# Kernel optimization log

Measured on AMD Instinct MI355X. Metric: run time of the kernel, lower is better.

The kernel has to match this reference:

```python
import jax, jax.numpy as jnp
import numpy as np

POLY_Q = 2.0  # normalizer='poly_2'
N_HEADS = 12
LN_EPS = 1e-5  # torch nn.LayerNorm default


def poly_norm(x, q=POLY_Q):
    # Newton solve for c such that sum_k 1/(-x-c)^q == 1, row-wise (last axis).
    c = jnp.min(-x, axis=-1, keepdims=True) - 1.0  # ensures -x - c >= 1
    for _ in range(6):
        base = -x - c
        poly_sum = jnp.sum(base ** (-q), axis=-1, keepdims=True)
        poly_sum_der = q * jnp.sum(base ** (-(q + 1.0)), axis=-1, keepdims=True)
        c = c - (poly_sum - 1.0) / (poly_sum_der + 1e-8)
    return (-x - c) ** (-q)


def layer_norm(x, g, b, eps=LN_EPS):
    m = jnp.mean(x, axis=-1, keepdims=True)
    v = jnp.mean((x - m) ** 2, axis=-1, keepdims=True)
    return (x - m) * jax.lax.rsqrt(v + eps) * g + b


def setup_inputs() -> dict:
    key = jax.random.key(0)
    B, S, D, M = 2, 1024, 768, 3072
    ks = jax.random.split(key, 8)
    sd = 1.0 / np.sqrt(D)
    sm = 1.0 / np.sqrt(M)
    return {
        "x": jax.random.normal(ks[0], (B, S, D), dtype=jnp.float32),
        "ln1_g": jnp.ones((D,), jnp.float32),
        "ln1_b": jnp.zeros((D,), jnp.float32),
        "wq": jax.random.normal(ks[1], (D, D), jnp.float32) * sd,
        "bq": jnp.zeros((D,), jnp.float32),
        "wk": jax.random.normal(ks[2], (D, D), jnp.float32) * sd,
        "bk": jnp.zeros((D,), jnp.float32),
        "wv": jax.random.normal(ks[3], (D, D), jnp.float32) * sd,
        "bv": jnp.zeros((D,), jnp.float32),
        "wo": jax.random.normal(ks[4], (D, D), jnp.float32) * sd,
        "bo": jnp.zeros((D,), jnp.float32),
        "ln2_g": jnp.ones((D,), jnp.float32),
        "ln2_b": jnp.zeros((D,), jnp.float32),
        "w1": jax.random.normal(ks[5], (D, M), jnp.float32) * sd,
        "b1": jnp.zeros((M,), jnp.float32),
        "w2": jax.random.normal(ks[6], (M, D), jnp.float32) * sm,
        "b2": jnp.zeros((D,), jnp.float32),
    }


def reference(x, ln1_g, ln1_b, wq, bq, wk, bk, wv, bv, wo, bo,
              ln2_g, ln2_b, w1, b1, w2, b2):
    B, S, D = x.shape
    H = N_HEADS
    Dh = D // H
    # --- pre-LN self-attention with poly normalizer ---
    y = layer_norm(x, ln1_g, ln1_b)
    q = (y @ wq + bq).reshape(B, S, H, Dh) / jnp.sqrt(jnp.float32(Dh))
    k = (y @ wk + bk).reshape(B, S, H, Dh)
    v = (y @ wv + bv).reshape(B, S, H, Dh)
    scores = jnp.einsum('bqhd,bkhd->bhqk', q, k)  # [B,H,S,S]
    attn_w = poly_norm(scores)
    attn = jnp.einsum('bhqk,bkhd->bqhd', attn_w, v).reshape(B, S, D)
    x1 = x + attn @ wo + bo  # residual 1
    # --- MLP block ---
    y2 = layer_norm(x1, ln2_g, ln2_b)
    h = jax.nn.gelu(y2 @ w1 + b1, approximate=False)  # torch GELU = exact erf
    out = x1 + h @ w2 + b2  # residual 2
    return out
```

## Files before the change

kernel.cpp:

```cpp
#include <hip/hip_runtime.h>

#define DEV __device__ __forceinline__

typedef unsigned short u16;
typedef __attribute__((ext_vector_type(8))) short bf16x8;
typedef __attribute__((ext_vector_type(4))) float f32x4;
typedef __attribute__((ext_vector_type(4))) unsigned int u32x4;

DEV u16 f2bf(float f) {
  union { float f; unsigned u; } un; un.f = f;
  unsigned r = un.u + 0x7fffu + ((un.u >> 16) & 1u);
  return (u16)(r >> 16);
}

DEV void gload16(const void* g, void* l) {
  __builtin_amdgcn_global_load_lds((const __attribute__((address_space(1))) void*)g,
                                   (__attribute__((address_space(3))) void*)l, 16, 0, 0);
}

template <int N>
DEV void vm_wait() { asm volatile("s_waitcnt vmcnt(%0)" :: "n"(N) : "memory"); }

DEV float blk_sum(float v, volatile float* sb) {
#pragma unroll
  for (int o = 32; o; o >>= 1) v += __shfl_xor(v, o);
  __syncthreads();
  if ((threadIdx.x & 63) == 0) sb[threadIdx.x >> 6] = v;
  __syncthreads();
  return sb[0] + sb[1] + sb[2] + sb[3];
}

__global__ __launch_bounds__(256) void ln_kernel(const float* __restrict__ x,
                                                 const float* __restrict__ g,
                                                 const float* __restrict__ b,
                                                 u16* __restrict__ y) {
  __shared__ float sb[4];
  const size_t row = blockIdx.x;
  const float* xr = x + row * 768;
  const int t = threadIdx.x;
  float v0 = xr[t], v1 = xr[t + 256], v2 = xr[t + 512];
  float mean = blk_sum(v0 + v1 + v2, sb) * (1.0f / 768.0f);
  float d0 = v0 - mean, d1 = v1 - mean, d2 = v2 - mean;
  float var = blk_sum(d0 * d0 + d1 * d1 + d2 * d2, sb) * (1.0f / 768.0f);
  float inv = rsqrtf(var + 1e-5f);
  u16* yr = y + row * 768;
  yr[t]       = f2bf(d0 * inv * g[t]       + b[t]);
  yr[t + 256] = f2bf(d1 * inv * g[t + 256] + b[t + 256]);
  yr[t + 512] = f2bf(d2 * inv * g[t + 512] + b[t + 512]);
}

__global__ __launch_bounds__(256) void wt_transpose(const float* __restrict__ in,
                                                    u16* __restrict__ out, int K, int N) {
  __shared__ float tile[32][33];
  const int tx = threadIdx.x & 31, ty = threadIdx.x >> 5;
  const int n0 = blockIdx.x * 32, k0 = blockIdx.y * 32;
#pragma unroll
  for (int i = 0; i < 4; i++)
    tile[ty + 8 * i][tx] = in[(size_t)(k0 + ty + 8 * i) * N + n0 + tx];
  __syncthreads();
#pragma unroll
  for (int i = 0; i < 4; i++)
    out[(size_t)(n0 + ty + 8 * i) * K + k0 + tx] = f2bf(tile[tx][ty + 8 * i]);
}

__global__ __launch_bounds__(256) void v_transpose(const u16* __restrict__ qkv,
                                                   u16* __restrict__ vT) {
  __shared__ u16 tile[32][33];
  const int tx = threadIdx.x & 31, ty = threadIdx.x >> 5;
  const int z = blockIdx.z, b = z / 12, h = z % 12;
  const int s0 = blockIdx.x * 32, d0 = blockIdx.y * 32;
#pragma unroll
  for (int i = 0; i < 4; i++)
    tile[ty + 8 * i][tx] =
        qkv[(size_t)(b * 1024 + s0 + ty + 8 * i) * 2304 + 1536 + h * 64 + d0 + tx];
  __syncthreads();
#pragma unroll
  for (int i = 0; i < 4; i++)
    vT[(size_t)(z * 64 + d0 + ty + 8 * i) * 1024 + s0 + tx] = tile[tx][ty + 8 * i];
}

__global__ __launch_bounds__(512) void fused_attn(const u16* __restrict__ qkv,
                                                  const u16* __restrict__ vT,
                                                  u16* __restrict__ attn) {
  __shared__ __align__(16) u16 wlds[16 * 1024];

  const int tid = threadIdx.x;
  const int w = tid >> 6, l = tid & 63;
  const int g = l >> 4, lr = l & 15;
  const int bh = blockIdx.y, b = bh / 12, h = bh % 12;
  const int q0 = blockIdx.x * 16;

  const u16* qrow = qkv + (size_t)(b * 1024 + q0 + lr) * 2304 + h * 64;
  const u16* krow = qkv + (size_t)(b * 1024 + w * 128 + lr) * 2304 + 768 + h * 64;

  bf16x8 af[2];
  af[0] = *(const bf16x8*)(qrow + g * 8);
  af[1] = *(const bf16x8*)(qrow + 32 + g * 8);

  f32x4 acc[8];
#pragma unroll
  for (int n = 0; n < 8; n++) acc[n] = (f32x4){0.f, 0.f, 0.f, 0.f};

#pragma unroll
  for (int n = 0; n < 8; n++) {
    bf16x8 b0 = *(const bf16x8*)(krow + n * 16 * 2304 + g * 8);
    bf16x8 b1 = *(const bf16x8*)(krow + n * 16 * 2304 + 32 + g * 8);
    acc[n] = __builtin_amdgcn_mfma_f32_16x16x32_bf16(af[0], b0, acc[n], 0, 0, 0);
    acc[n] = __builtin_amdgcn_mfma_f32_16x16x32_bf16(af[1], b1, acc[n], 0, 0, 0);
  }

#pragma unroll
  for (int n = 0; n < 8; n++)
#pragma unroll
    for (int r = 0; r < 4; r++) {
      int row = g * 4 + r;
      int col = w * 128 + n * 16 + lr;
      unsigned off = (unsigned)(row * 2048 + col * 2);
      off ^= (unsigned)(row & 7) << 4;
      *(u16*)((char*)wlds + off) = f2bf(acc[n][r]);
    }
  __syncthreads();

  const int crow = tid >> 5, l32 = tid & 31;
  const unsigned cswz = (unsigned)(crow & 7) << 4;
  const unsigned cbase = (unsigned)(crow * 2048 + l32 * 64);
  float xs[32];
#pragma unroll
  for (int j = 0; j < 4; j++) {
    u32x4 raw = *(const u32x4*)((const char*)wlds + ((cbase + j * 16u) ^ cswz));
#pragma unroll
    for (int e = 0; e < 4; e++) {
      union { unsigned u; float f; } lo, hi;
      lo.u = raw[e] << 16;
      hi.u = raw[e] & 0xffff0000u;
      xs[j * 8 + e * 2] = lo.f;
      xs[j * 8 + e * 2 + 1] = hi.f;
    }
  }

  float mx = xs[0];
#pragma unroll
  for (int i = 1; i < 32; i++) mx = fmaxf(mx, xs[i]);
#pragma unroll
  for (int o = 1; o < 32; o <<= 1) mx = fmaxf(mx, __shfl_xor(mx, o));
  float c = -mx - 1.0f;

#pragma unroll 1
  for (int it = 0; it < 6; it++) {
    float s2 = 0.f, s3 = 0.f;
#pragma unroll
    for (int i = 0; i < 32; i++) {
      float rr = __builtin_amdgcn_rcpf(-(xs[i] + c));
      float r2 = rr * rr;
      s2 += r2;
      s3 = fmaf(r2, rr, s3);
    }
#pragma unroll
    for (int o = 1; o < 32; o <<= 1) {
      s2 += __shfl_xor(s2, o);
      s3 += __shfl_xor(s3, o);
    }
    c -= (s2 - 1.0f) * __builtin_amdgcn_rcpf(2.0f * s3 + 1e-8f);
  }

#pragma unroll
  for (int j = 0; j < 4; j++) {
    u32x4 outv;
#pragma unroll
    for (int e = 0; e < 4; e++) {
      float r0 = __builtin_amdgcn_rcpf(-(xs[j * 8 + e * 2] + c));
      float r1 = __builtin_amdgcn_rcpf(-(xs[j * 8 + e * 2 + 1] + c));
      outv[e] = (unsigned)f2bf(r0 * r0) | ((unsigned)f2bf(r1 * r1) << 16);
    }
    *(u32x4*)((char*)wlds + ((cbase + j * 16u) ^ cswz)) = outv;
  }
  __syncthreads();

  if (w < 4) {
    const int nf = w;
    const u16* vrow = vT + (size_t)(bh * 64 + nf * 16 + lr) * 1024;
    const unsigned swz = (unsigned)(lr & 7) << 4;
    const unsigned abase = (unsigned)(lr * 2048);
    f32x4 oacc = (f32x4){0.f, 0.f, 0.f, 0.f};
#pragma unroll
    for (int ks = 0; ks < 32; ks++) {
      bf16x8 afr = *(const bf16x8*)((const char*)wlds +
                                    ((abase + (unsigned)(ks * 64 + g * 16)) ^ swz));
      bf16x8 bfr = *(const bf16x8*)(vrow + ks * 32 + g * 8);
      oacc = __builtin_amdgcn_mfma_f32_16x16x32_bf16(afr, bfr, oacc, 0, 0, 0);
    }
    u16* orow = attn + (size_t)(b * 1024 + q0 + g * 4) * 768 + h * 64 + nf * 16 + lr;
#pragma unroll
    for (int r = 0; r < 4; r++) orow[(size_t)r * 768] = f2bf(oacc[r]);
  }
}

__global__ __launch_bounds__(256) void splitk_reduce(const float* __restrict__ p,
                                                     const float* __restrict__ bias,
                                                     const float* __restrict__ res,
                                                     float* __restrict__ out) {
  const size_t S = 2048ull * 768;
  size_t i = ((size_t)blockIdx.x * 256 + threadIdx.x) * 4;
  f32x4 v = *(const f32x4*)&p[i];
  v += *(const f32x4*)&p[i + S];
  v += *(const f32x4*)&p[i + 2 * S];
  v += *(const f32x4*)&p[i + 3 * S];
  int col = (int)(i % 768);
  v += *(const f32x4*)&bias[col];
  v += *(const f32x4*)&res[i];
  *(f32x4*)&out[i] = v;
}

template <int BM, int WN, int EPI>
__global__ __launch_bounds__(256) void gemm_bt(
    const u16* __restrict__ A, int lda, long long sAb, long long sAh,
    const u16* __restrict__ B0, const u16* __restrict__ B1, const u16* __restrict__ B2,
    int ldb, long long sBb, long long sBh,
    void* __restrict__ Cv, int ldc, long long sCb, long long sCh,
    const float* __restrict__ bias0, const float* __restrict__ bias1,
    const float* __restrict__ bias2, const float* __restrict__ res, int K) {
  constexpr int WCOL = (BM == 128) ? 2 : 4;
  constexpr int BN = WCOL * WN * 16;
  constexpr int NA = BM / 64;
  constexpr int NB = BN / 64;
  constexpr int LT = NA + NB;
  __shared__ __align__(16) u16 lds_a[3][BM * 32];
  __shared__ __align__(16) u16 lds_b[3][BN * 32];

  const int zb = blockIdx.z / 12, zh = blockIdx.z % 12;
  A += zb * sAb + zh * sAh;

  const int colbase = blockIdx.y * BN;
  const u16* B = B0;
  const float* bias = bias0;
  int biasoff = 0;
  float qscale = 1.0f;
  if (EPI == 0) {
    int sel = colbase / 768;
    B = (sel == 0) ? B0 : ((sel == 1) ? B1 : B2);
    bias = (sel == 0) ? bias0 : ((sel == 1) ? bias1 : bias2);
    biasoff = sel * 768;
    qscale = (sel == 0) ? 0.125f : 1.0f;
  }
  B += zb * sBb + zh * sBh;

  const int tid = threadIdx.x;
  const size_t ldab = (size_t)lda * 2, ldbb = (size_t)ldb * 2;
  const char* Abase = (const char*)(A + (size_t)blockIdx.x * BM * lda);
  const char* Bbase = (const char*)(B + (size_t)(colbase - biasoff) * ldb);

  const char* ap[NA];
  const char* bp[NB];
#pragma unroll
  for (int j = 0; j < NA; j++) {
    int lin = (j * 256 + tid) * 16;
    ap[j] = Abase + (size_t)(lin >> 6) * ldab + (lin & 63);
  }
#pragma unroll
  for (int j = 0; j < NB; j++) {
    int lin = (j * 256 + tid) * 16;
    bp[j] = Bbase + (size_t)(lin >> 6) * ldbb + (lin & 63);
  }

  auto stage = [&](int buf) {
#pragma unroll
    for (int j = 0; j < NA; j++) {
      gload16(ap[j], (char*)&lds_a[buf][0] + (j * 256 + tid) * 16);
      ap[j] += 64;
    }
#pragma unroll
    for (int j = 0; j < NB; j++) {
      gload16(bp[j], (char*)&lds_b[buf][0] + (j * 256 + tid) * 16);
      bp[j] += 64;
    }
  };

  f32x4 acc[4][WN];
#pragma unroll
  for (int m = 0; m < 4; m++)
#pragma unroll
    for (int n = 0; n < WN; n++) acc[m][n] = (f32x4){0.f, 0.f, 0.f, 0.f};

  const int w = tid >> 6, l = tid & 63;
  const int wm = (BM == 128) ? (w >> 1) : 0;
  const int wn = (BM == 128) ? (w & 1) : w;
  const int lr = l & 15, kg = l >> 4;

  const int nt = K / 32;
  stage(0);
  if (nt > 1) stage(1);

  for (int t = 0; t < nt; ++t) {
    const int buf = t % 3;
    if (t + 2 < nt) {
      stage((t + 2) % 3);
      vm_wait<2 * LT>();
    } else if (t + 1 < nt) {
      vm_wait<LT>();
    } else {
      vm_wait<0>();
    }
    __builtin_amdgcn_sched_barrier(0);
    __builtin_amdgcn_s_barrier();
    __builtin_amdgcn_sched_barrier(0);

    bf16x8 af[4], bfr[WN];
#pragma unroll
    for (int m = 0; m < 4; m++)
      af[m] = *(const bf16x8*)&lds_a[buf][(wm * 64 + m * 16 + lr) * 32 + kg * 8];
#pragma unroll
    for (int n = 0; n < WN; n++)
      bfr[n] = *(const bf16x8*)&lds_b[buf][(wn * WN * 16 + n * 16 + lr) * 32 + kg * 8];
#pragma unroll
    for (int m = 0; m < 4; m++)
#pragma unroll
      for (int n = 0; n < WN; n++)
        acc[m][n] = __builtin_amdgcn_mfma_f32_16x16x32_bf16(af[m], bfr[n], acc[m][n], 0, 0, 0);

    __builtin_amdgcn_sched_barrier(0);
    __builtin_amdgcn_s_barrier();
    __builtin_amdgcn_sched_barrier(0);
  }

  const int row0 = blockIdx.x * BM + ((BM == 128) ? wm * 64 : 0) + kg * 4;
  const int colb = colbase + wn * WN * 16;
  float* Cf = (float*)Cv + (size_t)zb * sCb + (size_t)zh * sCh;
  u16* Cu = (u16*)Cv + (size_t)zb * sCb + (size_t)zh * sCh;
#pragma unroll
  for (int m = 0; m < 4; m++) {
#pragma unroll
    for (int n = 0; n < WN; n++) {
#pragma unroll
      for (int r = 0; r < 4; r++) {
        int row = row0 + m * 16 + r;
        int col = colb + n * 16 + lr;
        size_t idx = (size_t)row * ldc + col;
        float v = acc[m][n][r];
        if (EPI == 0) {
          Cu[idx] = f2bf((v + bias[col - biasoff]) * qscale);
        } else if (EPI == 1) {
          Cf[idx] = v;
        } else if (EPI == 2) {
          Cu[idx] = f2bf(v);
        } else if (EPI == 3) {
          Cf[idx] = v + bias[col] + res[idx];
        } else {
          v += bias[col];
          Cu[idx] = f2bf(0.5f * v * (1.0f + erff(v * 0.70710678118654752f)));
        }
      }
    }
  }
}

extern "C" void kernel_launch(void* const* d_in, const int* in_sizes, int n_in,
                              void* d_out, int out_size, void* d_ws, size_t ws_size,
                              hipStream_t stream) {
  const float* x     = (const float*)d_in[0];
  const float* ln1_g = (const float*)d_in[1];
  const float* ln1_b = (const float*)d_in[2];
  const float* wq    = (const float*)d_in[3];
  const float* bq    = (const float*)d_in[4];
  const float* wk    = (const float*)d_in[5];
  const float* bk    = (const float*)d_in[6];
  const float* wv    = (const float*)d_in[7];
  const float* bv    = (const float*)d_in[8];
  const float* wo    = (const float*)d_in[9];
  const float* bo    = (const float*)d_in[10];
  const float* ln2_g = (const float*)d_in[11];
  const float* ln2_b = (const float*)d_in[12];
  const float* w1    = (const float*)d_in[13];
  const float* b1    = (const float*)d_in[14];
  const float* w2    = (const float*)d_in[15];
  const float* b2    = (const float*)d_in[16];
  float* out = (float*)d_out;

  char* p = (char*)d_ws;
  auto alloc = [&](size_t n) { char* r = p; p += (n + 255) & ~(size_t)255; return r; };
  u16*   qkv    = (u16*)  alloc(2048ull * 2304 * 2);
  u16*   y1     = (u16*)  alloc(2048ull * 768 * 2);
  u16*   vT     = (u16*)  alloc(24ull * 64 * 1024 * 2);
  u16*   attn   = (u16*)  alloc(2048ull * 768 * 2);
  float* x1     = (float*)alloc(2048ull * 768 * 4);
  u16*   y2     = (u16*)  alloc(2048ull * 768 * 2);
  u16*   hbuf   = (u16*)  alloc(2048ull * 3072 * 2);
  float* pbuf   = (float*)alloc(4ull * 2048 * 768 * 4);
  u16*   wq_t   = (u16*)  alloc(768ull * 768 * 2);
  u16*   wk_t   = (u16*)  alloc(768ull * 768 * 2);
  u16*   wv_t   = (u16*)  alloc(768ull * 768 * 2);
  u16*   wo_t   = (u16*)  alloc(768ull * 768 * 2);
  u16*   w1_t   = (u16*)  alloc(3072ull * 768 * 2);
  u16*   w2_t   = (u16*)  alloc(768ull * 3072 * 2);
  (void)in_sizes; (void)n_in; (void)out_size; (void)ws_size;

  wt_transpose<<<dim3(24, 24), 256, 0, stream>>>(wq, wq_t, 768, 768);
  wt_transpose<<<dim3(24, 24), 256, 0, stream>>>(wk, wk_t, 768, 768);
  wt_transpose<<<dim3(24, 24), 256, 0, stream>>>(wv, wv_t, 768, 768);
  wt_transpose<<<dim3(24, 24), 256, 0, stream>>>(wo, wo_t, 768, 768);
  wt_transpose<<<dim3(96, 24), 256, 0, stream>>>(w1, w1_t, 768, 3072);
  wt_transpose<<<dim3(24, 96), 256, 0, stream>>>(w2, w2_t, 3072, 768);

  ln_kernel<<<2048, 256, 0, stream>>>(x, ln1_g, ln1_b, y1);

  gemm_bt<128, 4, 0><<<dim3(16, 18, 1), 256, 0, stream>>>(
      y1, 768, 0, 0, wq_t, wk_t, wv_t, 768, 0, 0, qkv, 2304, 0, 0, bq, bk, bv, nullptr, 768);

  v_transpose<<<dim3(32, 2, 24), 256, 0, stream>>>(qkv, vT);

  fused_attn<<<dim3(64, 24), 512, 0, stream>>>(qkv, vT, attn);

  gemm_bt<64, 2, 3><<<dim3(32, 6, 1), 256, 0, stream>>>(
      attn, 768, 0, 0, wo_t, nullptr, nullptr, 768, 0, 0, x1, 768, 0, 0,
      bo, nullptr, nullptr, x, 768);

  ln_kernel<<<2048, 256, 0, stream>>>(x1, ln2_g, ln2_b, y2);

  gemm_bt<128, 4, 4><<<dim3(16, 24, 1), 256, 0, stream>>>(
      y2, 768, 0, 0, w1_t, nullptr, nullptr, 768, 0, 0, hbuf, 3072, 0, 0,
      b1, nullptr, nullptr, nullptr, 768);

  gemm_bt<64, 2, 1><<<dim3(32, 6, 4), 256, 0, stream>>>(
      hbuf, 3072, 0, 768LL, w2_t, nullptr, nullptr, 3072, 0, 768LL,
      pbuf, 768, 0, 1572864LL, nullptr, nullptr, nullptr, nullptr, 768);

  splitk_reduce<<<1536, 256, 0, stream>>>(pbuf, b2, x1, out);
}
```

Baseline: 182.7 us.

## Merge weight transposes into one launch and fuse V transpose into QKV epilogue

Replaces six separate weight-transpose launches with one kernel that maps a flat block index to the right weight matrix. It also removes the V-transpose kernel: the QKV GEMM's V-column blocks now write bias-added V directly in transposed [b,h,d,s] layout into vT. This saves launch overhead and an extra read and write pass over V. In exchange the transposed epilogue stores are strided and uncoalesced, and the vT pointer is passed through the float res argument.

```diff
diff --git a/kernel.cpp b/kernel.cpp
--- a/kernel.cpp
+++ b/kernel.cpp
@@ -49,11 +49,32 @@
   yr[t + 512] = f2bf(d2 * inv * g[t + 512] + b[t + 512]);
 }
 
-__global__ __launch_bounds__(256) void wt_transpose(const float* __restrict__ in,
-                                                    u16* __restrict__ out, int K, int N) {
+__global__ __launch_bounds__(256) void wt_all(
+    const float* __restrict__ wq, const float* __restrict__ wk,
+    const float* __restrict__ wv, const float* __restrict__ wo,
+    const float* __restrict__ w1, const float* __restrict__ w2,
+    u16* __restrict__ oq, u16* __restrict__ ok, u16* __restrict__ ov,
+    u16* __restrict__ oo, u16* __restrict__ o1, u16* __restrict__ o2) {
   __shared__ float tile[32][33];
+  const int id = blockIdx.x;
+  const float* in;
+  u16* out;
+  int K, N, t, nx;
+  if (id < 2304) {
+    int s = id / 576;
+    t = id % 576;
+    K = 768; N = 768; nx = 24;
+    in  = (s == 0) ? wq : (s == 1) ? wk : (s == 2) ? wv : wo;
+    out = (s == 0) ? oq : (s == 1) ? ok : (s == 2) ? ov : oo;
+  } else if (id < 4608) {
+    t = id - 2304; in = w1; out = o1; K = 768; N = 3072; nx = 96;
+  } else {
+    t = id - 4608; in = w2; out = o2; K = 3072; N = 768; nx = 24;
+  }
+  const int yt = (nx == 96) ? (t / 96) : (t / 24);
+  const int xt = t - yt * nx;
+  const int n0 = xt * 32, k0 = yt * 32;
   const int tx = threadIdx.x & 31, ty = threadIdx.x >> 5;
-  const int n0 = blockIdx.x * 32, k0 = blockIdx.y * 32;
 #pragma unroll
   for (int i = 0; i < 4; i++)
     tile[ty + 8 * i][tx] = in[(size_t)(k0 + ty + 8 * i) * N + n0 + tx];
@@ -61,22 +82,6 @@
 #pragma unroll
   for (int i = 0; i < 4; i++)
     out[(size_t)(n0 + ty + 8 * i) * K + k0 + tx] = f2bf(tile[tx][ty + 8 * i]);
-}
-
-__global__ __launch_bounds__(256) void v_transpose(const u16* __restrict__ qkv,
-                                                   u16* __restrict__ vT) {
-  __shared__ u16 tile[32][33];
-  const int tx = threadIdx.x & 31, ty = threadIdx.x >> 5;
-  const int z = blockIdx.z, b = z / 12, h = z % 12;
-  const int s0 = blockIdx.x * 32, d0 = blockIdx.y * 32;
-#pragma unroll
-  for (int i = 0; i < 4; i++)
-    tile[ty + 8 * i][tx] =
-        qkv[(size_t)(b * 1024 + s0 + ty + 8 * i) * 2304 + 1536 + h * 64 + d0 + tx];
-  __syncthreads();
-#pragma unroll
-  for (int i = 0; i < 4; i++)
-    vT[(size_t)(z * 64 + d0 + ty + 8 * i) * 1024 + s0 + tx] = tile[tx][ty + 8 * i];
 }
 
 __global__ __launch_bounds__(512) void fused_attn(const u16* __restrict__ qkv,
@@ -235,8 +240,9 @@
   const float* bias = bias0;
   int biasoff = 0;
   float qscale = 1.0f;
+  int sel = 0;
   if (EPI == 0) {
-    int sel = colbase / 768;
+    sel = colbase / 768;
     B = (sel == 0) ? B0 : ((sel == 1) ? B1 : B2);
     bias = (sel == 0) ? bias0 : ((sel == 1) ? bias1 : bias2);
     biasoff = sel * 768;
@@ -326,6 +332,28 @@
   const int colb = colbase + wn * WN * 16;
   float* Cf = (float*)Cv + (size_t)zb * sCb + (size_t)zh * sCh;
   u16* Cu = (u16*)Cv + (size_t)zb * sCb + (size_t)zh * sCh;
+
+  if (EPI == 0 && sel == 2) {
+    u16* vTp = (u16*)res;
+#pragma unroll
+    for (int m = 0; m < 4; m++) {
+#pragma unroll
+      for (int n = 0; n < WN; n++) {
+#pragma unroll
+        for (int r = 0; r < 4; r++) {
+          int row = row0 + m * 16 + r;
+          int col = colb + n * 16 + lr;
+          int cv = col - 1536;
+          int bb = row >> 10, ss = row & 1023;
+          int hh = cv >> 6, dd = cv & 63;
+          vTp[(size_t)((bb * 12 + hh) * 64 + dd) * 1024 + ss] =
+              f2bf(acc[m][n][r] + bias[cv]);
+        }
+      }
+    }
+    return;
+  }
+
 #pragma unroll
   for (int m = 0; m < 4; m++) {
 #pragma unroll
@@ -393,19 +421,14 @@
   u16*   w2_t   = (u16*)  alloc(768ull * 3072 * 2);
   (void)in_sizes; (void)n_in; (void)out_size; (void)ws_size;
 
-  wt_transpose<<<dim3(24, 24), 256, 0, stream>>>(wq, wq_t, 768, 768);
-  wt_transpose<<<dim3(24, 24), 256, 0, stream>>>(wk, wk_t, 768, 768);
-  wt_transpose<<<dim3(24, 24), 256, 0, stream>>>(wv, wv_t, 768, 768);
-  wt_transpose<<<dim3(24, 24), 256, 0, stream>>>(wo, wo_t, 768, 768);
-  wt_transpose<<<dim3(96, 24), 256, 0, stream>>>(w1, w1_t, 768, 3072);
-  wt_transpose<<<dim3(24, 96), 256, 0, stream>>>(w2, w2_t, 3072, 768);
+  wt_all<<<6912, 256, 0, stream>>>(wq, wk, wv, wo, w1, w2,
+                                   wq_t, wk_t, wv_t, wo_t, w1_t, w2_t);
 
   ln_kernel<<<2048, 256, 0, stream>>>(x, ln1_g, ln1_b, y1);
 
   gemm_bt<128, 4, 0><<<dim3(16, 18, 1), 256, 0, stream>>>(
-      y1, 768, 0, 0, wq_t, wk_t, wv_t, 768, 0, 0, qkv, 2304, 0, 0, bq, bk, bv, nullptr, 768);
-
-  v_transpose<<<dim3(32, 2, 24), 256, 0, stream>>>(qkv, vT);
+      y1, 768, 0, 0, wq_t, wk_t, wv_t, 768, 0, 0, qkv, 2304, 0, 0,
+      bq, bk, bv, (const float*)vT, 768);
 
   fused_attn<<<dim3(64, 24), 512, 0, stream>>>(qkv, vT, attn);
 
```

Result: faster. 170.2 us (-6.9%).
